# Kernel tuning notes

Hardware: AMD Instinct MI355X
Metric: run time of the kernel (lower is better)

Reference implementation:

```python
import jax, jax.numpy as jnp
import numpy as np
from jax import lax

N = 50000
C = 8
HW = 11
E = 800000
BD = 4
LIN_DIM = C * (HW - 2) * (HW - 2) + BD  # 652
HID = 256
OUT = 5
EPS = 1e-5


def _layernorm(h, g, b):
    mu = jnp.mean(h, axis=-1, keepdims=True)
    var = jnp.var(h, axis=-1, keepdims=True)
    return (h - mu) * lax.rsqrt(var + EPS) * g + b


def setup_inputs() -> dict:
    key = jax.random.key(0)
    ks = jax.random.split(key, 20)
    x = jax.random.normal(ks[0], (N, C, HW, HW), dtype=jnp.float32)
    bd_pred = jax.random.normal(ks[1], (N, BD), dtype=jnp.float32)
    src = jax.random.randint(ks[2], (E,), 0, N)
    dst = jax.random.randint(ks[3], (E,), 0, N)
    dst = jnp.where(src == dst, (dst + 1) % N, dst)  # no self loops
    edge_index = jnp.stack([src, dst]).astype(jnp.int64)
    s = 0.02
    p = {
        'conv_self_w': jax.random.normal(ks[4], (C, C, 3, 3), jnp.float32) * s,
        'conv_self_b': jnp.zeros((C,), jnp.float32),
        'lin_w': jax.random.normal(ks[5], (HID, LIN_DIM), jnp.float32) * s,
        'lin_b': jnp.zeros((HID,), jnp.float32),
        'lin_self_w': jax.random.normal(ks[6], (HID, LIN_DIM), jnp.float32) * s,
        'lin_self_b': jnp.zeros((HID,), jnp.float32),
        'sage_l_w': jax.random.normal(ks[7], (3, HID, HID), jnp.float32) * s,
        'sage_l_b': jnp.zeros((3, HID), jnp.float32),
        'sage_r_w': jax.random.normal(ks[8], (3, HID, HID), jnp.float32) * s,
        'ln_g': jnp.ones((2, HID), jnp.float32),
        'ln_b': jnp.zeros((2, HID), jnp.float32),
        'mp1_w': jax.random.normal(ks[9], (HID, HID), jnp.float32) * s,
        'mp1_b': jnp.zeros((HID,), jnp.float32),
        'mp2_w': jax.random.normal(ks[10], (OUT, HID), jnp.float32) * s,
        'mp2_b': jnp.zeros((OUT,), jnp.float32),
    }
    return dict(x=x, bd_pred=bd_pred, edge_index=edge_index, **p)


def reference(x, bd_pred, edge_index, conv_self_w, conv_self_b, lin_w, lin_b,
              lin_self_w, lin_self_b, sage_l_w, sage_l_b, sage_r_w,
              ln_g, ln_b, mp1_w, mp1_b, mp2_w, mp2_b):
    n = x.shape[0]
    src, dst = edge_index[0], edge_index[1]

    # CustomConv layer 0: conv_self -> flatten -> hstack(bd_pred) -> relu -> two linears
    h = lax.conv_general_dilated(x, conv_self_w, (1, 1), 'VALID',
                                 dimension_numbers=('NCHW', 'OIHW', 'NCHW'))
    h = h + conv_self_b[None, :, None, None]
    h = jnp.concatenate([h.reshape(n, -1), bd_pred], axis=1)  # [N, 652]
    h = jax.nn.relu(h)
    self_x = h @ lin_self_w.T + lin_self_b
    neigh = h @ lin_w.T + lin_b
    h = self_x + jax.ops.segment_sum(neigh[src], dst, num_segments=n)  # aggr='add'

    # in-degree for SAGEConv mean aggregation
    deg = jax.ops.segment_sum(jnp.ones((src.shape[0],), h.dtype), dst, num_segments=n)
    deg = jnp.maximum(deg, 1.0)[:, None]

    emb = h
    for i in range(3):  # SAGEConv layers 1..3
        mean_agg = jax.ops.segment_sum(h[src], dst, num_segments=n) / deg
        h = mean_agg @ sage_l_w[i].T + sage_l_b[i] + h @ sage_r_w[i].T
        emb = h
        h = jax.nn.relu(h)
        # dropout p=0.25 is identity in eval mode
        if i != 2:
            h = _layernorm(h, ln_g[i], ln_b[i])

    z = h @ mp1_w.T + mp1_b
    z = z @ mp2_w.T + mp2_b
    return emb, jax.nn.log_softmax(z, axis=1)
```

## Files before the change

### kernel.cpp

```cpp
#include <hip/hip_runtime.h>
#include <hip/hip_bf16.h>
#include <stdint.h>

#define NN 50000
#define EE 800000

typedef unsigned short u16;
typedef __attribute__((ext_vector_type(4))) float f32x4;
typedef __attribute__((ext_vector_type(8))) short bf16x8;

__device__ __forceinline__ float bu2f(u16 u){ return __uint_as_float(((unsigned)u)<<16); }
__device__ __forceinline__ u16 f2bu(float f){
  unsigned u = __float_as_uint(f);
  u += 0x7fffu + ((u>>16)&1u);
  return (u16)(u>>16);
}

__global__ void sniff_kernel(const int* __restrict__ e, const u16* __restrict__ xu,
                             int* __restrict__ flags){
  __shared__ int nz, cnt;
  int t = threadIdx.x;
  if (t == 0){ nz = 0; cnt = 0; }
  __syncthreads();
  if (e[2*t + 1] != 0) atomicOr(&nz, 1);
  u16 u = xu[2*t];
  int ef = (u >> 7) & 0xFF;
  int ok = (u == 0) || (ef >= 118 && ef <= 132);
  atomicAdd(&cnt, ok);
  __syncthreads();
  if (t == 0){ flags[0] = (nz == 0) ? 1 : 0; flags[1] = (cnt >= 200) ? 1 : 0; }
}

__global__ void convert_edges_kernel(const void* __restrict__ ep, int* __restrict__ outp,
                                     const int* __restrict__ flags, int total){
  int i = blockIdx.x*256 + threadIdx.x;
  if (i >= total) return;
  if (flags[0]) outp[i] = (int)((const long long*)ep)[i];
  else          outp[i] = ((const int*)ep)[i];
}

struct CanonTab {
  const void* src[15];
  void*       dst[15];
  int rows[15];
  int sk[15];
  int dk[15];
  int tobf[15];
};

__global__ __launch_bounds__(256) void canon_params_kernel(CanonTab tab, const int* __restrict__ flags){
  int a = blockIdx.y;
  int isbf = flags[1];
  int rows = tab.rows[a], sk = tab.sk[a], dk = tab.dk[a], tobf = tab.tobf[a];
  int n = rows * dk;
  int base = (blockIdx.x*256 + threadIdx.x) * 8;
  if (base >= n) return;
  #pragma unroll
  for (int uu = 0; uu < 8; uu++){
    int i = base + uu;
    if (i >= n) break;
    int r = i / dk, c = i - r*dk;
    float v = 0.f;
    if (c < sk){
      size_t si = (size_t)r*sk + c;
      v = isbf ? bu2f(((const u16*)tab.src[a])[si]) : ((const float*)tab.src[a])[si];
    }
    if (tobf) ((u16*)tab.dst[a])[i] = f2bu(v);
    else      ((float*)tab.dst[a])[i] = v;
  }
}

__global__ __launch_bounds__(256) void conv_relu_kernel(
    const void* __restrict__ xraw, const void* __restrict__ bdraw,
    const float* __restrict__ cw, const float* __restrict__ cb,
    const int* __restrict__ flags, u16* __restrict__ h0){
  __shared__ float xs[968];
  __shared__ float wsm[576];
  __shared__ float bs[8];
  int n = blockIdx.x, t = threadIdx.x;
  int isbf = flags[1];
  if (isbf){
    const ushort4* xp = (const ushort4*)((const u16*)xraw + (size_t)n*968);
    if (t < 242){ ushort4 u = xp[t]; xs[4*t]=bu2f(u.x); xs[4*t+1]=bu2f(u.y); xs[4*t+2]=bu2f(u.z); xs[4*t+3]=bu2f(u.w); }
  } else {
    const float4* xp = (const float4*)((const float*)xraw + (size_t)n*968);
    if (t < 242){ float4 u = xp[t]; xs[4*t]=u.x; xs[4*t+1]=u.y; xs[4*t+2]=u.z; xs[4*t+3]=u.w; }
  }
  if (t < 144){ float4 u = ((const float4*)cw)[t]; wsm[4*t]=u.x; wsm[4*t+1]=u.y; wsm[4*t+2]=u.z; wsm[4*t+3]=u.w; }
  if (t < 8) bs[t] = cb[t];
  __syncthreads();
  u16* outr = h0 + (size_t)n*672;
  for (int base = 0; base < 672; base += 256){
    int j = base + t;
    if (j >= 672) continue;
    float v; int outcol;
    if (j < 648){
      int co = j & 7, pos = j >> 3;
      int oi = pos/9, oj = pos%9;
      outcol = co*81 + pos;
      float acc = bs[co];
      const float* wp = wsm + co*72;
      const float* xb = xs + oi*11 + oj;
      #pragma unroll
      for (int ci=0; ci<8; ci++)
        #pragma unroll
        for (int ki=0; ki<3; ki++)
          #pragma unroll
          for (int kj=0; kj<3; kj++)
            acc += xb[ci*121 + ki*11 + kj] * wp[ci*9 + ki*3 + kj];
      v = acc;
    } else if (j < 652){
      outcol = j;
      int jj = j - 648;
      v = isbf ? bu2f(((const u16*)bdraw)[(size_t)n*4 + jj]) : ((const float*)bdraw)[(size_t)n*4 + jj];
    } else {
      outcol = j; v = 0.f;
    }
    outr[outcol] = f2bu(fmaxf(v, 0.f));
  }
}

__global__ void deg_kernel(const int* __restrict__ dst, int* __restrict__ degI, int E){
  int e = blockIdx.x*256 + threadIdx.x;
  if (e < E) atomicAdd(&degI[dst[e]], 1);
}
__global__ void invdeg_kernel(const int* __restrict__ degI, float* __restrict__ inv, int n){
  int i = blockIdx.x*256 + threadIdx.x;
  if (i < n){ int d = degI[i]; inv[i] = 1.0f / (float)(d > 1 ? d : 1); }
}

__global__ __launch_bounds__(1024) void scan_kernel(const int* __restrict__ degI,
                                                    int* __restrict__ rowptr,
                                                    int* __restrict__ cursor, int n){
  __shared__ int warp_sums[16];
  __shared__ int carry;
  int t = threadIdx.x;
  if (t == 0) carry = 0;
  __syncthreads();
  for (int base = 0; base < n; base += 1024){
    int i = base + t;
    int v = (i < n) ? degI[i] : 0;
    int s = v;
    #pragma unroll
    for (int off = 1; off < 64; off <<= 1){ int u = __shfl_up(s, off); if ((t & 63) >= off) s += u; }
    if ((t & 63) == 63) warp_sums[t >> 6] = s;
    __syncthreads();
    if (t < 16){
      int wsv = warp_sums[t];
      #pragma unroll
      for (int off = 1; off < 16; off <<= 1){ int u = __shfl_up(wsv, off); if (t >= off) wsv += u; }
      warp_sums[t] = wsv;
    }
    __syncthreads();
    int block_off = (t >= 64) ? warp_sums[(t >> 6) - 1] : 0;
    int excl = carry + block_off + s - v;
    if (i < n){ rowptr[i] = excl; cursor[i] = excl; }
    int total = warp_sums[15];
    __syncthreads();
    if (t == 0) carry += total;
    __syncthreads();
  }
  if (t == 0) rowptr[n] = carry;
}

__global__ void bucket_kernel(const int* __restrict__ esrc, const int* __restrict__ edst,
                              int* __restrict__ cursor, int* __restrict__ ebuc, int E){
  int e = blockIdx.x*256 + threadIdx.x;
  if (e < E){ int pos = atomicAdd(&cursor[edst[e]], 1); ebuc[pos] = esrc[e]; }
}

__global__ __launch_bounds__(256) void gather_agg_kernel(
    const u16* __restrict__ src_feat, const u16* __restrict__ addbase,
    const float* __restrict__ scale, u16* __restrict__ outp,
    const int* __restrict__ rowptr, const int* __restrict__ ebuc){
  int wid = threadIdx.x >> 6, lane = threadIdx.x & 63;
  int n = blockIdx.x*4 + wid;
  if (n >= NN) return;
  int beg = rowptr[n], end = rowptr[n+1];
  float a0=0.f,a1=0.f,a2=0.f,a3=0.f;
  float b0=0.f,b1=0.f,b2=0.f,b3=0.f;
  int j = beg;
  for (; j + 1 < end; j += 2){
    int s0 = ebuc[j], s1 = ebuc[j+1];
    ushort4 v0 = *(const ushort4*)(src_feat + (size_t)s0*256 + lane*4);
    ushort4 v1 = *(const ushort4*)(src_feat + (size_t)s1*256 + lane*4);
    a0 += bu2f(v0.x); a1 += bu2f(v0.y); a2 += bu2f(v0.z); a3 += bu2f(v0.w);
    b0 += bu2f(v1.x); b1 += bu2f(v1.y); b2 += bu2f(v1.z); b3 += bu2f(v1.w);
  }
  if (j < end){
    ushort4 v0 = *(const ushort4*)(src_feat + (size_t)ebuc[j]*256 + lane*4);
    a0 += bu2f(v0.x); a1 += bu2f(v0.y); a2 += bu2f(v0.z); a3 += bu2f(v0.w);
  }
  float sc = scale ? scale[n] : 1.f;
  a0 = (a0+b0)*sc; a1 = (a1+b1)*sc; a2 = (a2+b2)*sc; a3 = (a3+b3)*sc;
  if (addbase){
    ushort4 b = *(const ushort4*)(addbase + (size_t)n*256 + lane*4);
    a0 += bu2f(b.x); a1 += bu2f(b.y); a2 += bu2f(b.z); a3 += bu2f(b.w);
  }
  ushort4 o; o.x = f2bu(a0); o.y = f2bu(a1); o.z = f2bu(a2); o.w = f2bu(a3);
  *(ushort4*)(outp + (size_t)n*256 + lane*4) = o;
}

__global__ __launch_bounds__(256) void gemm_mfma_kernel(
    const u16* __restrict__ A1, int lda1, const u16* __restrict__ W1, int K1,
    const u16* __restrict__ A2, int lda2, const u16* __restrict__ W2, int K2,
    const float* __restrict__ bias,
    u16* __restrict__ out_bf,
    void* __restrict__ out_emb,
    u16* __restrict__ out_relu_bf,
    const int* __restrict__ flags, int M){
  __shared__ u16 Asm[128][40];
  __shared__ u16 Wsm[128][40];
  int t = threadIdx.x;
  int wave = t >> 6, lane = t & 63;
  int wr = wave >> 1, wc = wave & 1;
  int m0 = blockIdx.x << 7;
  int o0 = blockIdx.y << 7;
  int lrow = t >> 1;
  int lk8  = (t & 1) << 3;
  int fr = lane & 15;
  int fk = (lane >> 4) << 3;
  f32x4 acc[4][4] = {};

  for (int pass = 0; pass < 2; ++pass){
    const u16* A; const u16* W; int K, lda;
    if (pass == 0){ A = A1; W = W1; K = K1; lda = lda1; }
    else { if (!A2) break; A = A2; W = W2; K = K2; lda = lda2; }
    for (int k0 = 0; k0 < K; k0 += 32){
      int gm = m0 + lrow;
      int4 av0 = make_int4(0,0,0,0), av1 = av0;
      if (gm < M){
        const int4* ap = (const int4*)(A + (size_t)gm*lda + k0 + lk8);
        av0 = ap[0];
        av1 = ap[2];
      }
      const int4* wp = (const int4*)(W + (size_t)(o0 + lrow)*K + k0 + lk8);
      int4 wv0 = wp[0];
      int4 wv1 = wp[2];
      *(int4*)&Asm[lrow][lk8]      = av0;
      *(int4*)&Asm[lrow][lk8+16]   = av1;
      *(int4*)&Wsm[lrow][lk8]      = wv0;
      *(int4*)&Wsm[lrow][lk8+16]   = wv1;
      __syncthreads();
      bf16x8 af[4], wf[4];
      #pragma unroll
      for (int i = 0; i < 4; i++) af[i] = *(const bf16x8*)&Asm[wr*64 + i*16 + fr][fk];
      #pragma unroll
      for (int jj = 0; jj < 4; jj++) wf[jj] = *(const bf16x8*)&Wsm[wc*64 + jj*16 + fr][fk];
      #pragma unroll
      for (int i = 0; i < 4; i++)
        #pragma unroll
        for (int jj = 0; jj < 4; jj++)
          acc[i][jj] = __builtin_amdgcn_mfma_f32_16x16x32_bf16(af[i], wf[jj], acc[i][jj], 0, 0, 0);
      __syncthreads();
    }
  }
  int isbf = flags[1];
  int fg = lane >> 4;
  #pragma unroll
  for (int i = 0; i < 4; i++){
    int rbase = m0 + wr*64 + i*16 + fg*4;
    #pragma unroll
    for (int jj = 0; jj < 4; jj++){
      int col = o0 + wc*64 + jj*16 + fr;
      float bv = bias[col];
      #pragma unroll
      for (int r = 0; r < 4; r++){
        int row = rbase + r;
        if (row < M){
          float v = acc[i][jj][r] + bv;
          size_t off = (size_t)row*256 + col;
          if (out_bf)   out_bf[off] = f2bu(v);
          if (out_emb){
            if (isbf) ((u16*)out_emb)[off] = f2bu(v);
            else      ((float*)out_emb)[off] = v;
          }
          if (out_relu_bf) out_relu_bf[off] = f2bu(fmaxf(v, 0.f));
        }
      }
    }
  }
}

__global__ __launch_bounds__(256) void relu_ln_kernel(
    const u16* __restrict__ inb, u16* __restrict__ outb,
    const float* __restrict__ g, const float* __restrict__ b){
  __shared__ float rs[4], rs2[4];
  int n = blockIdx.x, t = threadIdx.x;
  float v = fmaxf(bu2f(inb[(size_t)n*256 + t]), 0.f);
  float s = v, s2 = v*v;
  #pragma unroll
  for (int off = 1; off < 64; off <<= 1){ s += __shfl_xor(s, off); s2 += __shfl_xor(s2, off); }
  if ((t & 63) == 0){ rs[t>>6] = s; rs2[t>>6] = s2; }
  __syncthreads();
  float S  = rs[0]+rs[1]+rs[2]+rs[3];
  float S2 = rs2[0]+rs2[1]+rs2[2]+rs2[3];
  float mu  = S * (1.f/256.f);
  float var = S2 * (1.f/256.f) - mu*mu;
  float inv = rsqrtf(var + 1e-5f);
  outb[(size_t)n*256 + t] = f2bu((v - mu) * inv * g[t] + b[t]);
}

__global__ __launch_bounds__(256) void head_kernel(
    const u16* __restrict__ z1, const float* __restrict__ w2, const float* __restrict__ b2,
    void* __restrict__ outbase, size_t out_off, const int* __restrict__ flags, int M){
  __shared__ float wsm[1280];
  __shared__ float bs[5];
  int t = threadIdx.x;
  for (int i = t; i < 320; i += 256){
    float4 u = ((const float4*)w2)[i];
    wsm[4*i]=u.x; wsm[4*i+1]=u.y; wsm[4*i+2]=u.z; wsm[4*i+3]=u.w;
  }
  if (t < 5) bs[t] = b2[t];
  __syncthreads();
  int n = blockIdx.x*256 + t;
  if (n >= M) return;
  const u16* zp = z1 + (size_t)n*256;
  float acc[5];
  #pragma unroll
  for (int o = 0; o < 5; o++) acc[o] = bs[o];
  for (int k = 0; k < 256; k += 4){
    ushort4 zu = *(const ushort4*)(zp + k);
    float z0 = bu2f(zu.x), z1f = bu2f(zu.y), z2 = bu2f(zu.z), z3 = bu2f(zu.w);
    #pragma unroll
    for (int o = 0; o < 5; o++){
      const float* w = wsm + o*256 + k;
      acc[o] += z0*w[0] + z1f*w[1] + z2*w[2] + z3*w[3];
    }
  }
  float mx = acc[0];
  #pragma unroll
  for (int o = 1; o < 5; o++) mx = fmaxf(mx, acc[o]);
  float se = 0.f;
  #pragma unroll
  for (int o = 0; o < 5; o++) se += expf(acc[o] - mx);
  float lse = mx + logf(se);
  int isbf = flags[1];
  if (isbf){
    u16* op = (u16*)outbase + out_off + (size_t)n*5;
    #pragma unroll
    for (int o = 0; o < 5; o++) op[o] = f2bu(acc[o] - lse);
  } else {
    float* op = (float*)outbase + out_off + (size_t)n*5;
    #pragma unroll
    for (int o = 0; o < 5; o++) op[o] = acc[o] - lse;
  }
}

extern "C" void kernel_launch(void* const* d_in, const int* in_sizes, int n_in,
                              void* d_out, int out_size, void* d_ws, size_t ws_size,
                              hipStream_t stream){
  (void)in_sizes; (void)n_in; (void)out_size; (void)ws_size;
  const void* x    = d_in[0];
  const void* bd   = d_in[1];
  const void* eraw = d_in[2];

  char* ws = (char*)d_ws;
  const size_t OFF_H0 = 0;
  const size_t OFF_A  = OFF_H0 + (size_t)NN*672*2;
  const size_t OFF_B  = OFF_A  + (size_t)NN*256*2;
  const size_t OFF_C  = OFF_B  + (size_t)NN*256*2;
  const size_t OFF_DEG= OFF_C  + (size_t)NN*256*2;
  const size_t OFF_INV= OFF_DEG + (size_t)NN*4;
  const size_t OFF_EDG= OFF_INV + (size_t)NN*4;
  const size_t OFF_RP = OFF_EDG + (size_t)2*EE*4;
  const size_t OFF_CUR= OFF_RP  + (size_t)(NN+16)*4;
  const size_t OFF_EBU= OFF_CUR + (size_t)NN*4;
  const size_t OFF_FLG= OFF_EBU + (size_t)EE*4;
  const size_t OFF_PRM= OFF_FLG + 256;

  u16*   h0   = (u16*)(ws + OFF_H0);
  u16*   bufA = (u16*)(ws + OFF_A);
  u16*   bufB = (u16*)(ws + OFF_B);
  u16*   bufC = (u16*)(ws + OFF_C);
  int*   degI = (int*)(ws + OFF_DEG);
  float* invd = (float*)(ws + OFF_INV);
  int*   edg  = (int*)(ws + OFF_EDG);
  int*   rowp = (int*)(ws + OFF_RP);
  int*   curs = (int*)(ws + OFF_CUR);
  int*   ebuc = (int*)(ws + OFF_EBU);
  int*   flg  = (int*)(ws + OFF_FLG);
  char*  prm  = ws + OFF_PRM;
  const int* esrc = edg;
  const int* edst = edg + EE;

  static const int crows[15] = {1,1,256,1,256,1,1,1,1,1,1,1,1,1,1};
  static const int csk[15]   = {576,8,652,256,652,256,196608,768,196608,512,512,65536,256,1280,5};
  static const int cdk[15]   = {576,8,672,256,672,256,196608,768,196608,512,512,65536,256,1280,5};
  static const int ctobf[15] = {0,0,1,0,1,0,1,0,1,0,0,1,0,0,0};
  CanonTab tab;
  size_t po = 0;
  void* dsts[15];
  for (int i = 0; i < 15; i++){
    tab.src[i] = d_in[3+i];
    tab.rows[i] = crows[i]; tab.sk[i] = csk[i]; tab.dk[i] = cdk[i]; tab.tobf[i] = ctobf[i];
    dsts[i] = prm + po;
    tab.dst[i] = dsts[i];
    size_t bytes = (size_t)crows[i]*cdk[i] * (ctobf[i] ? 2 : 4);
    po += (bytes + 63) & ~(size_t)63;
  }
  const float* c_cw  = (const float*)dsts[0];
  const float* c_cb  = (const float*)dsts[1];
  const u16*   c_lw  = (const u16*)dsts[2];
  const float* c_lb  = (const float*)dsts[3];
  const u16*   c_lsw = (const u16*)dsts[4];
  const float* c_lsb = (const float*)dsts[5];
  const u16*   c_slw = (const u16*)dsts[6];
  const float* c_slb = (const float*)dsts[7];
  const u16*   c_srw = (const u16*)dsts[8];
  const float* c_lng = (const float*)dsts[9];
  const float* c_lnb = (const float*)dsts[10];
  const u16*   c_m1w = (const u16*)dsts[11];
  const float* c_m1b = (const float*)dsts[12];
  const float* c_m2w = (const float*)dsts[13];
  const float* c_m2b = (const float*)dsts[14];

  hipMemsetAsync(degI, 0, (size_t)NN*4, stream);
  sniff_kernel<<<1, 256, 0, stream>>>((const int*)eraw, (const u16*)x, flg);
  {
    dim3 cgrid(96, 15);
    canon_params_kernel<<<cgrid, 256, 0, stream>>>(tab, flg);
  }
  convert_edges_kernel<<<(2*EE + 255)/256, 256, 0, stream>>>(eraw, edg, flg, 2*EE);
  conv_relu_kernel<<<NN, 256, 0, stream>>>(x, bd, c_cw, c_cb, flg, h0);
  deg_kernel<<<(EE + 255)/256, 256, 0, stream>>>(edst, degI, EE);
  invdeg_kernel<<<(NN + 255)/256, 256, 0, stream>>>(degI, invd, NN);
  scan_kernel<<<1, 1024, 0, stream>>>(degI, rowp, curs, NN);
  bucket_kernel<<<(EE + 255)/256, 256, 0, stream>>>(esrc, edst, curs, ebuc, EE);

  dim3 ggrid((NN + 127)/128, 2);
  const int agrid = (NN + 3)/4;
  gemm_mfma_kernel<<<ggrid, 256, 0, stream>>>(h0, 672, c_lsw, 672,
      nullptr, 0, nullptr, 0, c_lsb, bufA, nullptr, nullptr, flg, NN);
  gemm_mfma_kernel<<<ggrid, 256, 0, stream>>>(h0, 672, c_lw, 672,
      nullptr, 0, nullptr, 0, c_lb, bufB, nullptr, nullptr, flg, NN);
  gather_agg_kernel<<<agrid, 256, 0, stream>>>(bufB, bufA, nullptr, bufA, rowp, ebuc);

  for (int i = 0; i < 3; i++){
    gather_agg_kernel<<<agrid, 256, 0, stream>>>(bufA, nullptr, invd, bufC, rowp, ebuc);
    const u16*   L  = c_slw + (size_t)i*256*256;
    const float* Lb = c_slb + (size_t)i*256;
    const u16*   R  = c_srw + (size_t)i*256*256;
    if (i < 2){
      gemm_mfma_kernel<<<ggrid, 256, 0, stream>>>(bufC, 256, L, 256,
          bufA, 256, R, 256, Lb, bufB, nullptr, nullptr, flg, NN);
      relu_ln_kernel<<<NN, 256, 0, stream>>>(bufB, bufA,
          c_lng + (size_t)i*256, c_lnb + (size_t)i*256);
    } else {
      gemm_mfma_kernel<<<ggrid, 256, 0, stream>>>(bufC, 256, L, 256,
          bufA, 256, R, 256, Lb, nullptr, d_out, bufB, flg, NN);
    }
  }
  gemm_mfma_kernel<<<ggrid, 256, 0, stream>>>(bufB, 256, c_m1w, 256,
      nullptr, 0, nullptr, 0, c_m1b, bufC, nullptr, nullptr, flg, NN);
  head_kernel<<<(NN + 255)/256, 256, 0, stream>>>(bufC, c_m2w, c_m2b,
      d_out, (size_t)NN*256, flg, NN);
}
```

Before: 1.016 ms.

## Deepen GEMM K-tile to 64 and register-block the 3x3 conv

The MFMA GEMM now stages 64-wide K slices in shared memory, which halves the number of barrier pairs per tile and issues two MFMA sub-steps per load. The padded input width grows from 672 to 704 so K divides evenly by 64, at the cost of extra zero padding and a larger h0 buffer. The conv kernel is also rewritten so each thread keeps its filter in registers and computes three adjacent outputs, reusing overlapping input loads. The costs are higher register pressure and more LDS per block, which may lower occupancy.

```diff
diff --git a/kernel.cpp b/kernel.cpp
--- a/kernel.cpp
+++ b/kernel.cpp
@@ -89,34 +89,38 @@
   if (t < 144){ float4 u = ((const float4*)cw)[t]; wsm[4*t]=u.x; wsm[4*t+1]=u.y; wsm[4*t+2]=u.z; wsm[4*t+3]=u.w; }
   if (t < 8) bs[t] = cb[t];
   __syncthreads();
-  u16* outr = h0 + (size_t)n*672;
-  for (int base = 0; base < 672; base += 256){
-    int j = base + t;
-    if (j >= 672) continue;
-    float v; int outcol;
-    if (j < 648){
-      int co = j & 7, pos = j >> 3;
-      int oi = pos/9, oj = pos%9;
-      outcol = co*81 + pos;
-      float acc = bs[co];
-      const float* wp = wsm + co*72;
-      const float* xb = xs + oi*11 + oj;
+  u16* outr = h0 + (size_t)n*704;
+  if (t < 216){
+    int co = t & 7;
+    int rowid = t >> 3;
+    int oi = rowid / 3;
+    int og = rowid - oi*3;
+    float wreg[72];
+    #pragma unroll
+    for (int q = 0; q < 72; q++) wreg[q] = wsm[co*72 + q];
+    float a0 = bs[co], a1 = a0, a2 = a0;
+    #pragma unroll
+    for (int ci = 0; ci < 8; ci++){
       #pragma unroll
-      for (int ci=0; ci<8; ci++)
-        #pragma unroll
-        for (int ki=0; ki<3; ki++)
-          #pragma unroll
-          for (int kj=0; kj<3; kj++)
-            acc += xb[ci*121 + ki*11 + kj] * wp[ci*9 + ki*3 + kj];
-      v = acc;
-    } else if (j < 652){
-      outcol = j;
-      int jj = j - 648;
-      v = isbf ? bu2f(((const u16*)bdraw)[(size_t)n*4 + jj]) : ((const float*)bdraw)[(size_t)n*4 + jj];
-    } else {
-      outcol = j; v = 0.f;
-    }
-    outr[outcol] = f2bu(fmaxf(v, 0.f));
+      for (int ki = 0; ki < 3; ki++){
+        const float* xb = xs + ci*121 + (oi+ki)*11 + og*3;
+        float x0=xb[0], x1=xb[1], x2=xb[2], x3=xb[3], x4=xb[4];
+        float w0=wreg[ci*9+ki*3+0], w1=wreg[ci*9+ki*3+1], w2=wreg[ci*9+ki*3+2];
+        a0 += x0*w0 + x1*w1 + x2*w2;
+        a1 += x1*w0 + x2*w1 + x3*w2;
+        a2 += x2*w0 + x3*w1 + x4*w2;
+      }
+    }
+    int colbase = co*81 + oi*9 + og*3;
+    outr[colbase+0] = f2bu(fmaxf(a0, 0.f));
+    outr[colbase+1] = f2bu(fmaxf(a1, 0.f));
+    outr[colbase+2] = f2bu(fmaxf(a2, 0.f));
+  } else if (t < 220){
+    int jj = t - 216;
+    float v = isbf ? bu2f(((const u16*)bdraw)[(size_t)n*4 + jj]) : ((const float*)bdraw)[(size_t)n*4 + jj];
+    outr[648 + jj] = f2bu(fmaxf(v, 0.f));
+  } else {
+    for (int c = 652 + (t - 220); c < 704; c += 36) outr[c] = 0;
   }
 }
 
@@ -209,8 +213,8 @@
     void* __restrict__ out_emb,
     u16* __restrict__ out_relu_bf,
     const int* __restrict__ flags, int M){
-  __shared__ u16 Asm[128][40];
-  __shared__ u16 Wsm[128][40];
+  __shared__ u16 Asm[128][72];
+  __shared__ u16 Wsm[128][72];
   int t = threadIdx.x;
   int wave = t >> 6, lane = t & 63;
   int wr = wave >> 1, wc = wave & 1;
@@ -219,39 +223,45 @@
   int lrow = t >> 1;
   int lk8  = (t & 1) << 3;
   int fr = lane & 15;
-  int fk = (lane >> 4) << 3;
+  int fkb = (lane >> 4) << 3;
   f32x4 acc[4][4] = {};
 
   for (int pass = 0; pass < 2; ++pass){
     const u16* A; const u16* W; int K, lda;
     if (pass == 0){ A = A1; W = W1; K = K1; lda = lda1; }
     else { if (!A2) break; A = A2; W = W2; K = K2; lda = lda2; }
-    for (int k0 = 0; k0 < K; k0 += 32){
+    for (int k0 = 0; k0 < K; k0 += 64){
       int gm = m0 + lrow;
-      int4 av0 = make_int4(0,0,0,0), av1 = av0;
+      int4 av0 = make_int4(0,0,0,0), av1 = av0, av2 = av0, av3 = av0;
       if (gm < M){
         const int4* ap = (const int4*)(A + (size_t)gm*lda + k0 + lk8);
-        av0 = ap[0];
-        av1 = ap[2];
+        av0 = ap[0]; av1 = ap[2]; av2 = ap[4]; av3 = ap[6];
       }
       const int4* wp = (const int4*)(W + (size_t)(o0 + lrow)*K + k0 + lk8);
-      int4 wv0 = wp[0];
-      int4 wv1 = wp[2];
+      int4 wv0 = wp[0], wv1 = wp[2], wv2 = wp[4], wv3 = wp[6];
       *(int4*)&Asm[lrow][lk8]      = av0;
       *(int4*)&Asm[lrow][lk8+16]   = av1;
+      *(int4*)&Asm[lrow][lk8+32]   = av2;
+      *(int4*)&Asm[lrow][lk8+48]   = av3;
       *(int4*)&Wsm[lrow][lk8]      = wv0;
       *(int4*)&Wsm[lrow][lk8+16]   = wv1;
+      *(int4*)&Wsm[lrow][lk8+32]   = wv2;
+      *(int4*)&Wsm[lrow][lk8+48]   = wv3;
       __syncthreads();
-      bf16x8 af[4], wf[4];
       #pragma unroll
-      for (int i = 0; i < 4; i++) af[i] = *(const bf16x8*)&Asm[wr*64 + i*16 + fr][fk];
-      #pragma unroll
-      for (int jj = 0; jj < 4; jj++) wf[jj] = *(const bf16x8*)&Wsm[wc*64 + jj*16 + fr][fk];
-      #pragma unroll
-      for (int i = 0; i < 4; i++)
+      for (int kk = 0; kk < 2; kk++){
+        int fk = kk*32 + fkb;
+        bf16x8 af[4], wf[4];
         #pragma unroll
-        for (int jj = 0; jj < 4; jj++)
-          acc[i][jj] = __builtin_amdgcn_mfma_f32_16x16x32_bf16(af[i], wf[jj], acc[i][jj], 0, 0, 0);
+        for (int i = 0; i < 4; i++) af[i] = *(const bf16x8*)&Asm[wr*64 + i*16 + fr][fk];
+        #pragma unroll
+        for (int jj = 0; jj < 4; jj++) wf[jj] = *(const bf16x8*)&Wsm[wc*64 + jj*16 + fr][fk];
+        #pragma unroll
+        for (int i = 0; i < 4; i++)
+          #pragma unroll
+          for (int jj = 0; jj < 4; jj++)
+            acc[i][jj] = __builtin_amdgcn_mfma_f32_16x16x32_bf16(af[i], wf[jj], acc[i][jj], 0, 0, 0);
+      }
       __syncthreads();
     }
   }
@@ -357,7 +367,7 @@
 
   char* ws = (char*)d_ws;
   const size_t OFF_H0 = 0;
-  const size_t OFF_A  = OFF_H0 + (size_t)NN*672*2;
+  const size_t OFF_A  = OFF_H0 + (size_t)NN*704*2;
   const size_t OFF_B  = OFF_A  + (size_t)NN*256*2;
   const size_t OFF_C  = OFF_B  + (size_t)NN*256*2;
   const size_t OFF_DEG= OFF_C  + (size_t)NN*256*2;
@@ -386,7 +396,7 @@
 
   static const int crows[15] = {1,1,256,1,256,1,1,1,1,1,1,1,1,1,1};
   static const int csk[15]   = {576,8,652,256,652,256,196608,768,196608,512,512,65536,256,1280,5};
-  static const int cdk[15]   = {576,8,672,256,672,256,196608,768,196608,512,512,65536,256,1280,5};
+  static const int cdk[15]   = {576,8,704,256,704,256,196608,768,196608,512,512,65536,256,1280,5};
   static const int ctobf[15] = {0,0,1,0,1,0,1,0,1,0,0,1,0,0,0};
   CanonTab tab;
   size_t po = 0;
@@ -430,9 +440,9 @@
 
   dim3 ggrid((NN + 127)/128, 2);
   const int agrid = (NN + 3)/4;
-  gemm_mfma_kernel<<<ggrid, 256, 0, stream>>>(h0, 672, c_lsw, 672,
+  gemm_mfma_kernel<<<ggrid, 256, 0, stream>>>(h0, 704, c_lsw, 704,
       nullptr, 0, nullptr, 0, c_lsb, bufA, nullptr, nullptr, flg, NN);
-  gemm_mfma_kernel<<<ggrid, 256, 0, stream>>>(h0, 672, c_lw, 672,
+  gemm_mfma_kernel<<<ggrid, 256, 0, stream>>>(h0, 704, c_lw, 704,
       nullptr, 0, nullptr, 0, c_lb, bufB, nullptr, nullptr, flg, NN);
   gather_agg_kernel<<<agrid, 256, 0, stream>>>(bufB, bufA, nullptr, bufA, rowp, ebuc);
 
```

Measured after the change: 899.8 us. -11.5%, faster.
